# Optimization experiments

Hardware: AMD Instinct MI355X
Metric: run time of the kernel (lower is better)

The kernel has to match this reference:

```python
import jax, jax.numpy as jnp
import numpy as np


def _layernorm(x, g, b, eps=1e-5):
    mu = jnp.mean(x, axis=-1, keepdims=True)
    var = jnp.mean(jnp.square(x - mu), axis=-1, keepdims=True)
    return (x - mu) * jax.lax.rsqrt(var + eps) * g + b


def setup_inputs() -> dict:
    key = jax.random.key(0)
    ks = jax.random.split(key, 8)
    B, S, E, K, H = 32, 64, 768, 36, 4
    w = 0.02
    return {
        "x": jax.random.normal(ks[0], (B, S, E), dtype=jnp.float32),
        "y": jax.random.normal(ks[1], (B * S, K, E), dtype=jnp.float32),
        "ln_gamma": jnp.ones((H, E), jnp.float32),
        "ln_beta": jnp.zeros((H, E), jnp.float32),
        "W1": jax.random.normal(ks[2], (H, E, E), dtype=jnp.float32) * w,
        "b1": jnp.zeros((H, E), jnp.float32),
        "W2x": jax.random.normal(ks[3], (H, E), dtype=jnp.float32) * w,  # first half of Linear(2E,1)
        "W2y": jax.random.normal(ks[4], (H, E), dtype=jnp.float32) * w,  # second half of Linear(2E,1)
        "b2": jnp.zeros((H,), jnp.float32),
        "Wm": jax.random.normal(ks[5], (H * E, E), dtype=jnp.float32) * w,
        "bm": jnp.zeros((E,), jnp.float32),
        "select_indegree_num": 36,
    }


def reference(x, y, ln_gamma, ln_beta, W1, b1, W2x, W2y, b2, Wm, bm, select_indegree_num):
    # x: [B,S,E], y: [B*S,K,E]; dropout layers are identity in eval mode.
    B, S, E = x.shape
    H = ln_gamma.shape[0]
    xf = x.reshape(B * S, E)
    outs = []
    for h in range(H):
        # shared linear1 (LayerNorm + Linear) applied to both x and y
        x_ = _layernorm(xf, ln_gamma[h], ln_beta[h]) @ W1[h] + b1[h]          # [BS,E]
        y_ = _layernorm(y, ln_gamma[h], ln_beta[h]) @ W1[h] + b1[h]           # [BS,K,E]
        logit = (x_ @ W2x[h])[:, None] + y_ @ W2y[h] + b2[h]                  # [BS,K]
        prob = jax.nn.softmax(logit, axis=1)                                   # softmax over neighbors
        a = jnp.einsum('nk,nke->ne', prob, y_)                                 # weighted sum, [BS,E]
        outs.append(jax.nn.gelu(xf + a))                                       # GELU(x + a)
    cat = jnp.concatenate(outs, axis=-1)                                       # [BS,H*E]
    res = jax.nn.gelu(cat @ Wm + bm).reshape(B, S, E)
    return x + res  # has_residual=True
```

## Files before the change

kernel.cpp:

```cpp
#include <hip/hip_runtime.h>
#include <hip/hip_bf16.h>

#define EE 768
#define HH 4
#define KK 36
#define BSN 2048

typedef __attribute__((ext_vector_type(8))) short short8;
typedef __attribute__((ext_vector_type(4))) short short4v;
typedef __attribute__((ext_vector_type(4))) float float4v;

__device__ inline short f2bf(float x){
  return __builtin_bit_cast(short, __float2bfloat16(x));
}
__device__ inline float bf2f(short s){
  return __bfloat162float(__builtin_bit_cast(__hip_bfloat16, s));
}
__device__ inline float gelu_tanh(float x){
  float t = tanhf(0.79788456080286536f * (x + 0.044715f * x * x * x));
  return 0.5f * x * (1.0f + t);
}

__global__ __launch_bounds__(256) void k_v(const float* __restrict__ W1,
                                           const float* __restrict__ W2y,
                                           const float* __restrict__ g,
                                           const float* __restrict__ b1,
                                           float* __restrict__ v,
                                           float* __restrict__ b1p){
  const int wid  = blockIdx.x * 4 + (threadIdx.x >> 6);
  const int lane = threadIdx.x & 63;
  const int h = wid / EE, e = wid % EE;
  const float* W  = W1 + ((size_t)h * EE + e) * EE;
  const float* wy = W2y + h * EE;
  float acc = 0.f;
  #pragma unroll
  for (int j = 0; j < 12; ++j){
    int f = lane + 64 * j;
    acc += W[f] * wy[f];
  }
  #pragma unroll
  for (int off = 32; off; off >>= 1) acc += __shfl_xor(acc, off);
  if (lane == 0) v[h * EE + e] = g[h * EE + e] * acc;

  int idx = blockIdx.x * 256 + threadIdx.x;
  if (idx < HH * EE) b1p[idx] = b1[idx];
}

__global__ __launch_bounds__(256) void k_b1p_acc(const float* __restrict__ W1,
                                                 const float* __restrict__ beta,
                                                 float* __restrict__ b1p){
  const int h   = blockIdx.x >> 6;
  const int ec0 = (blockIdx.x & 63) * 12;
  const float* W  = W1 + (size_t)h * EE * EE;
  const float* bt = beta + h * EE;
  const int f = threadIdx.x;
  float a0 = 0.f, a1 = 0.f, a2 = 0.f;
  #pragma unroll
  for (int e = ec0; e < ec0 + 12; ++e){
    float be = bt[e];
    const float* row = W + (size_t)e * EE;
    a0 += be * row[f];
    a1 += be * row[f + 256];
    a2 += be * row[f + 512];
  }
  atomicAdd(&b1p[h * EE + f],       a0);
  atomicAdd(&b1p[h * EE + f + 256], a1);
  atomicAdd(&b1p[h * EE + f + 512], a2);
}

__global__ __launch_bounds__(256) void k_tW1(const float* __restrict__ W1,
                                             const float* __restrict__ g,
                                             short* __restrict__ W1t){
  __shared__ float tile[32][33];
  const int h  = blockIdx.z;
  const int e0 = blockIdx.x * 32, f0 = blockIdx.y * 32;
  const int tx = threadIdx.x & 31, ty = threadIdx.x >> 5;
  const float* W = W1 + (size_t)h * EE * EE;
  #pragma unroll
  for (int i = 0; i < 4; ++i){
    int e = e0 + ty + 8 * i;
    tile[ty + 8 * i][tx] = W[(size_t)e * EE + f0 + tx] * g[h * EE + e];
  }
  __syncthreads();
  #pragma unroll
  for (int i = 0; i < 4; ++i){
    int f = f0 + ty + 8 * i;
    W1t[((size_t)h * EE + f) * EE + e0 + tx] = f2bf(tile[tx][ty + 8 * i]);
  }
}

__global__ __launch_bounds__(256) void k_tWm(const float* __restrict__ Wm,
                                             short* __restrict__ Wmt){
  __shared__ float tile[32][33];
  const int c0 = blockIdx.x * 32, f0 = blockIdx.y * 32;
  const int tx = threadIdx.x & 31, ty = threadIdx.x >> 5;
  #pragma unroll
  for (int i = 0; i < 4; ++i){
    tile[ty + 8 * i][tx] = Wm[(size_t)(c0 + ty + 8 * i) * EE + f0 + tx];
  }
  __syncthreads();
  #pragma unroll
  for (int i = 0; i < 4; ++i){
    Wmt[(size_t)(f0 + ty + 8 * i) * (HH * EE) + c0 + tx] = f2bf(tile[tx][ty + 8 * i]);
  }
}

__global__ __launch_bounds__(256, 2) void k_pass_y(const float* __restrict__ y,
                                                   const float* __restrict__ v,
                                                   short* __restrict__ p_y){
  __shared__ short yn_s[KK][EE];
  __shared__ float logits_s[KK][HH];
  __shared__ float prob_s[KK][HH];
  const int n = blockIdx.x;
  const int wave = threadIdx.x >> 6, lane = threadIdx.x & 63;

  float4v yv[9][3];
  #pragma unroll
  for (int i = 0; i < 9; ++i){
    const int k = wave + 4 * i;
    const float* yrow = y + ((size_t)n * KK + k) * EE;
    #pragma unroll
    for (int j = 0; j < 3; ++j)
      yv[i][j] = *(const float4v*)(yrow + 4 * lane + 256 * j);
  }

  float4v vreg[HH][3];
  #pragma unroll
  for (int h = 0; h < HH; ++h)
    #pragma unroll
    for (int j = 0; j < 3; ++j)
      vreg[h][j] = *(const float4v*)(v + h * EE + 4 * lane + 256 * j);

  #pragma unroll
  for (int i = 0; i < 9; ++i){
    const int k = wave + 4 * i;
    float s = 0.f, s2 = 0.f;
    #pragma unroll
    for (int j = 0; j < 3; ++j)
      #pragma unroll
      for (int c = 0; c < 4; ++c){ float t = yv[i][j][c]; s += t; s2 += t * t; }
    #pragma unroll
    for (int off = 32; off; off >>= 1){
      s  += __shfl_xor(s, off);
      s2 += __shfl_xor(s2, off);
    }
    const float mu = s * (1.f / EE);
    const float rs = rsqrtf(s2 * (1.f / EE) - mu * mu + 1e-5f);
    float d0 = 0.f, d1 = 0.f, d2 = 0.f, d3 = 0.f;
    #pragma unroll
    for (int j = 0; j < 3; ++j){
      short4v pk;
      #pragma unroll
      for (int c = 0; c < 4; ++c){
        float t = (yv[i][j][c] - mu) * rs;
        pk[c] = f2bf(t);
        d0 += t * vreg[0][j][c];
        d1 += t * vreg[1][j][c];
        d2 += t * vreg[2][j][c];
        d3 += t * vreg[3][j][c];
      }
      *(short4v*)(&yn_s[k][4 * lane + 256 * j]) = pk;
    }
    #pragma unroll
    for (int off = 32; off; off >>= 1){
      d0 += __shfl_xor(d0, off);
      d1 += __shfl_xor(d1, off);
      d2 += __shfl_xor(d2, off);
      d3 += __shfl_xor(d3, off);
    }
    if (lane == 0){
      logits_s[k][0] = d0; logits_s[k][1] = d1;
      logits_s[k][2] = d2; logits_s[k][3] = d3;
    }
  }
  __syncthreads();
  {
    const int h = wave;
    float l = (lane < KK) ? logits_s[lane][h] : -1e30f;
    float mx = l;
    #pragma unroll
    for (int off = 32; off; off >>= 1) mx = fmaxf(mx, __shfl_xor(mx, off));
    float ex = (lane < KK) ? __expf(l - mx) : 0.f;
    float sm = ex;
    #pragma unroll
    for (int off = 32; off; off >>= 1) sm += __shfl_xor(sm, off);
    if (lane < KK) prob_s[lane][h] = ex / sm;
  }
  __syncthreads();
  if (threadIdx.x < 192){
    const int e = 4 * threadIdx.x;
    float a[HH][4];
    #pragma unroll
    for (int h = 0; h < HH; ++h)
      #pragma unroll
      for (int c = 0; c < 4; ++c) a[h][c] = 0.f;
    #pragma unroll 4
    for (int k = 0; k < KK; ++k){
      short4v yp = *(const short4v*)(&yn_s[k][e]);
      float p0 = prob_s[k][0], p1 = prob_s[k][1], p2 = prob_s[k][2], p3 = prob_s[k][3];
      #pragma unroll
      for (int c = 0; c < 4; ++c){
        float t = bf2f(yp[c]);
        a[0][c] += p0 * t; a[1][c] += p1 * t; a[2][c] += p2 * t; a[3][c] += p3 * t;
      }
    }
    #pragma unroll
    for (int h = 0; h < HH; ++h){
      short4v pk;
      #pragma unroll
      for (int c = 0; c < 4; ++c) pk[c] = f2bf(a[h][c]);
      *(short4v*)(p_y + ((size_t)h * BSN + n) * EE + e) = pk;
    }
  }
}

template<int MODE>
__global__ __launch_bounds__(256) void k_gemm(const short* __restrict__ A,
                                              const short* __restrict__ Bt,
                                              const float* __restrict__ addv,
                                              const float* __restrict__ x,
                                              void* __restrict__ out,
                                              int Kdim, size_t strideA, size_t strideB){
  __shared__ short As[64][72];
  __shared__ short Bs[64][72];
  const int z = blockIdx.z;
  const short* Ah = A + strideA * z;
  const short* Bh = Bt + strideB * z;
  const float* addh = addv + (size_t)768 * z;

  const int tid = threadIdx.x;
  const int wave = tid >> 6, lane = tid & 63;
  const int quad = lane >> 4, l16 = lane & 15;
  const int m0 = blockIdx.x * 64, n0 = blockIdx.y * 64;
  const int r = tid >> 3, c8 = (tid & 7) * 8;

  float4v acc[4];
  #pragma unroll
  for (int t = 0; t < 4; ++t) acc[t] = (float4v){0.f, 0.f, 0.f, 0.f};

  const short* Ap0 = Ah + (size_t)(m0 + r) * Kdim + c8;
  const short* Ap1 = Ah + (size_t)(m0 + r + 32) * Kdim + c8;
  const short* Bp0 = Bh + (size_t)(n0 + r) * Kdim + c8;
  const short* Bp1 = Bh + (size_t)(n0 + r + 32) * Kdim + c8;

  for (int k0 = 0; k0 < Kdim; k0 += 64){
    short8 a0 = *(const short8*)(Ap0 + k0);
    short8 a1 = *(const short8*)(Ap1 + k0);
    short8 b0 = *(const short8*)(Bp0 + k0);
    short8 b1 = *(const short8*)(Bp1 + k0);
    __syncthreads();
    *(short8*)(&As[r][c8])      = a0;
    *(short8*)(&As[r + 32][c8]) = a1;
    *(short8*)(&Bs[r][c8])      = b0;
    *(short8*)(&Bs[r + 32][c8]) = b1;
    __syncthreads();
    #pragma unroll
    for (int kk = 0; kk < 64; kk += 32){
      short8 bf = *(const short8*)(&Bs[16 * wave + l16][kk + quad * 8]);
      #pragma unroll
      for (int t = 0; t < 4; ++t){
        short8 af = *(const short8*)(&As[16 * t + l16][kk + quad * 8]);
        acc[t] = __builtin_amdgcn_mfma_f32_16x16x32_bf16(af, bf, acc[t], 0, 0, 0);
      }
    }
  }

  const int f = n0 + 16 * wave + l16;
  const float add = addh[f];
  #pragma unroll
  for (int t = 0; t < 4; ++t){
    #pragma unroll
    for (int rr = 0; rr < 4; ++rr){
      const int m = m0 + 16 * t + quad * 4 + rr;
      const float val = acc[t][rr] + add;
      const float xf = x[(size_t)m * EE + f];
      if (MODE == 0){
        ((short*)out)[(size_t)m * (HH * EE) + 768 * z + f] = f2bf(gelu_tanh(xf + val));
      } else {
        ((float*)out)[(size_t)m * EE + f] = xf + gelu_tanh(val);
      }
    }
  }
}

extern "C" void kernel_launch(void* const* d_in, const int* in_sizes, int n_in,
                              void* d_out, int out_size, void* d_ws, size_t ws_size,
                              hipStream_t stream){
  const float* x    = (const float*)d_in[0];
  const float* y    = (const float*)d_in[1];
  const float* g    = (const float*)d_in[2];
  const float* beta = (const float*)d_in[3];
  const float* W1   = (const float*)d_in[4];
  const float* b1   = (const float*)d_in[5];
  const float* W2y  = (const float*)d_in[7];
  const float* Wm   = (const float*)d_in[9];
  const float* bm   = (const float*)d_in[10];

  char* ws = (char*)d_ws;
  float* v    = (float*)(ws + 0);
  float* b1p  = (float*)(ws + 12288);
  short* W1t  = (short*)(ws + 24576);
  short* Wmt  = (short*)(ws + 4743168);
  short* p_y  = (short*)(ws + 9461760);
  short* catb = (short*)(ws + 22044672);
  float* out  = (float*)d_out;

  k_v<<<dim3(768), dim3(256), 0, stream>>>(W1, W2y, g, b1, v, b1p);
  k_b1p_acc<<<dim3(256), dim3(256), 0, stream>>>(W1, beta, b1p);
  k_tW1<<<dim3(24, 24, 4), dim3(256), 0, stream>>>(W1, g, W1t);
  k_tWm<<<dim3(96, 24), dim3(256), 0, stream>>>(Wm, Wmt);
  k_pass_y<<<dim3(2048), dim3(256), 0, stream>>>(y, v, p_y);
  k_gemm<0><<<dim3(32, 12, 4), dim3(256), 0, stream>>>(
      p_y, W1t, b1p, x, (void*)catb, 768, (size_t)2048 * 768, (size_t)768 * 768);
  k_gemm<1><<<dim3(32, 12, 1), dim3(256), 0, stream>>>(
      catb, Wmt, bm, x, (void*)out, 3072, (size_t)0, (size_t)0);
}
```

Measured before the change: 444.2 us.

## Fuse y-pass softmax and weighted sum into one wave with online softmax

Reworks k_pass_y so each wave handles one node and streams its 36 neighbor rows with a double-buffered register prefetch. It computes the logits and applies an online (running-max) softmax that accumulates the weighted sum in registers, replacing the shared-memory staging, the two block barriers and the separate softmax and reduction phases. The kernel now launches a quarter as many blocks. The cost is heavier register use (48 accumulators plus the buffers), per-neighbor serial rescaling, and less memory-level parallelism per wave, since loads are now issued only two rows ahead.

```diff
diff --git a/kernel.cpp b/kernel.cpp
--- a/kernel.cpp
+++ b/kernel.cpp
@@ -1,5 +1,6 @@
 #include <hip/hip_runtime.h>
 #include <hip/hip_bf16.h>
+#include <math.h>
 
 #define EE 768
 #define HH 4
@@ -105,24 +106,12 @@
   }
 }
 
-__global__ __launch_bounds__(256, 2) void k_pass_y(const float* __restrict__ y,
-                                                   const float* __restrict__ v,
-                                                   short* __restrict__ p_y){
-  __shared__ short yn_s[KK][EE];
-  __shared__ float logits_s[KK][HH];
-  __shared__ float prob_s[KK][HH];
-  const int n = blockIdx.x;
+__global__ __launch_bounds__(256) void k_pass_y(const float* __restrict__ y,
+                                                const float* __restrict__ v,
+                                                short* __restrict__ p_y){
   const int wave = threadIdx.x >> 6, lane = threadIdx.x & 63;
-
-  float4v yv[9][3];
-  #pragma unroll
-  for (int i = 0; i < 9; ++i){
-    const int k = wave + 4 * i;
-    const float* yrow = y + ((size_t)n * KK + k) * EE;
-    #pragma unroll
-    for (int j = 0; j < 3; ++j)
-      yv[i][j] = *(const float4v*)(yrow + 4 * lane + 256 * j);
-  }
+  const int n = blockIdx.x * 4 + wave;
+  const float* base = y + (size_t)n * KK * EE + 4 * lane;
 
   float4v vreg[HH][3];
   #pragma unroll
@@ -131,14 +120,40 @@
     for (int j = 0; j < 3; ++j)
       vreg[h][j] = *(const float4v*)(v + h * EE + 4 * lane + 256 * j);
 
-  #pragma unroll
-  for (int i = 0; i < 9; ++i){
-    const int k = wave + 4 * i;
+  float4v acc[HH][3];
+  #pragma unroll
+  for (int h = 0; h < HH; ++h)
+    #pragma unroll
+    for (int j = 0; j < 3; ++j)
+      acc[h][j] = (float4v){0.f, 0.f, 0.f, 0.f};
+  float m[HH], l[HH];
+  #pragma unroll
+  for (int h = 0; h < HH; ++h){ m[h] = -INFINITY; l[h] = 0.f; }
+
+  float4v bufA[3], bufB[3];
+  #pragma unroll
+  for (int j = 0; j < 3; ++j) bufA[j] = *(const float4v*)(base + 256 * j);
+  #pragma unroll
+  for (int j = 0; j < 3; ++j) bufB[j] = *(const float4v*)(base + EE + 256 * j);
+
+  #pragma unroll 2
+  for (int k = 0; k < KK; ++k){
+    float4v cur[3];
+    #pragma unroll
+    for (int j = 0; j < 3; ++j) cur[j] = bufA[j];
+    #pragma unroll
+    for (int j = 0; j < 3; ++j) bufA[j] = bufB[j];
+    if (k + 2 < KK){
+      const float* rp = base + (size_t)(k + 2) * EE;
+      #pragma unroll
+      for (int j = 0; j < 3; ++j) bufB[j] = *(const float4v*)(rp + 256 * j);
+    }
+
     float s = 0.f, s2 = 0.f;
     #pragma unroll
     for (int j = 0; j < 3; ++j)
       #pragma unroll
-      for (int c = 0; c < 4; ++c){ float t = yv[i][j][c]; s += t; s2 += t * t; }
+      for (int c = 0; c < 4; ++c){ float t = cur[j][c]; s += t; s2 += t * t; }
     #pragma unroll
     for (int off = 32; off; off >>= 1){
       s  += __shfl_xor(s, off);
@@ -146,70 +161,56 @@
     }
     const float mu = s * (1.f / EE);
     const float rs = rsqrtf(s2 * (1.f / EE) - mu * mu + 1e-5f);
-    float d0 = 0.f, d1 = 0.f, d2 = 0.f, d3 = 0.f;
+
+    float d[HH] = {0.f, 0.f, 0.f, 0.f};
+    #pragma unroll
+    for (int j = 0; j < 3; ++j)
+      #pragma unroll
+      for (int c = 0; c < 4; ++c){
+        float t = (cur[j][c] - mu) * rs;
+        cur[j][c] = t;
+        d[0] += t * vreg[0][j][c];
+        d[1] += t * vreg[1][j][c];
+        d[2] += t * vreg[2][j][c];
+        d[3] += t * vreg[3][j][c];
+      }
+    #pragma unroll
+    for (int off = 32; off; off >>= 1){
+      d[0] += __shfl_xor(d[0], off);
+      d[1] += __shfl_xor(d[1], off);
+      d[2] += __shfl_xor(d[2], off);
+      d[3] += __shfl_xor(d[3], off);
+    }
+
+    #pragma unroll
+    for (int h = 0; h < HH; ++h){
+      if (d[h] > m[h]){
+        float sc = __expf(m[h] - d[h]);
+        l[h] *= sc;
+        #pragma unroll
+        for (int j = 0; j < 3; ++j)
+          #pragma unroll
+          for (int c = 0; c < 4; ++c) acc[h][j][c] *= sc;
+        m[h] = d[h];
+      }
+      float w = __expf(d[h] - m[h]);
+      l[h] += w;
+      #pragma unroll
+      for (int j = 0; j < 3; ++j)
+        #pragma unroll
+        for (int c = 0; c < 4; ++c) acc[h][j][c] += w * cur[j][c];
+    }
+  }
+
+  #pragma unroll
+  for (int h = 0; h < HH; ++h){
+    const float inv = 1.f / l[h];
     #pragma unroll
     for (int j = 0; j < 3; ++j){
       short4v pk;
       #pragma unroll
-      for (int c = 0; c < 4; ++c){
-        float t = (yv[i][j][c] - mu) * rs;
-        pk[c] = f2bf(t);
-        d0 += t * vreg[0][j][c];
-        d1 += t * vreg[1][j][c];
-        d2 += t * vreg[2][j][c];
-        d3 += t * vreg[3][j][c];
-      }
-      *(short4v*)(&yn_s[k][4 * lane + 256 * j]) = pk;
-    }
-    #pragma unroll
-    for (int off = 32; off; off >>= 1){
-      d0 += __shfl_xor(d0, off);
-      d1 += __shfl_xor(d1, off);
-      d2 += __shfl_xor(d2, off);
-      d3 += __shfl_xor(d3, off);
-    }
-    if (lane == 0){
-      logits_s[k][0] = d0; logits_s[k][1] = d1;
-      logits_s[k][2] = d2; logits_s[k][3] = d3;
-    }
-  }
-  __syncthreads();
-  {
-    const int h = wave;
-    float l = (lane < KK) ? logits_s[lane][h] : -1e30f;
-    float mx = l;
-    #pragma unroll
-    for (int off = 32; off; off >>= 1) mx = fmaxf(mx, __shfl_xor(mx, off));
-    float ex = (lane < KK) ? __expf(l - mx) : 0.f;
-    float sm = ex;
-    #pragma unroll
-    for (int off = 32; off; off >>= 1) sm += __shfl_xor(sm, off);
-    if (lane < KK) prob_s[lane][h] = ex / sm;
-  }
-  __syncthreads();
-  if (threadIdx.x < 192){
-    const int e = 4 * threadIdx.x;
-    float a[HH][4];
-    #pragma unroll
-    for (int h = 0; h < HH; ++h)
-      #pragma unroll
-      for (int c = 0; c < 4; ++c) a[h][c] = 0.f;
-    #pragma unroll 4
-    for (int k = 0; k < KK; ++k){
-      short4v yp = *(const short4v*)(&yn_s[k][e]);
-      float p0 = prob_s[k][0], p1 = prob_s[k][1], p2 = prob_s[k][2], p3 = prob_s[k][3];
-      #pragma unroll
-      for (int c = 0; c < 4; ++c){
-        float t = bf2f(yp[c]);
-        a[0][c] += p0 * t; a[1][c] += p1 * t; a[2][c] += p2 * t; a[3][c] += p3 * t;
-      }
-    }
-    #pragma unroll
-    for (int h = 0; h < HH; ++h){
-      short4v pk;
-      #pragma unroll
-      for (int c = 0; c < 4; ++c) pk[c] = f2bf(a[h][c]);
-      *(short4v*)(p_y + ((size_t)h * BSN + n) * EE + e) = pk;
+      for (int c = 0; c < 4; ++c) pk[c] = f2bf(acc[h][j][c] * inv);
+      *(short4v*)(p_y + ((size_t)h * BSN + n) * EE + 4 * lane + 256 * j) = pk;
     }
   }
 }
@@ -309,7 +310,7 @@
   k_b1p_acc<<<dim3(256), dim3(256), 0, stream>>>(W1, beta, b1p);
   k_tW1<<<dim3(24, 24, 4), dim3(256), 0, stream>>>(W1, g, W1t);
   k_tWm<<<dim3(96, 24), dim3(256), 0, stream>>>(Wm, Wmt);
-  k_pass_y<<<dim3(2048), dim3(256), 0, stream>>>(y, v, p_y);
+  k_pass_y<<<dim3(512), dim3(256), 0, stream>>>(y, v, p_y);
   k_gemm<0><<<dim3(32, 12, 4), dim3(256), 0, stream>>>(
       p_y, W1t, b1p, x, (void*)catb, 768, (size_t)2048 * 768, (size_t)768 * 768);
   k_gemm<1><<<dim3(32, 12, 1), dim3(256), 0, stream>>>(
```

Result: no change. 444.0 us (-0.0%).
